# Kernel optimization log

Measured on AMD Instinct MI355X. Metric: run time of the kernel, lower is better.

The kernel has to match this reference:

```python
import jax, jax.numpy as jnp
import numpy as np

LMAX = 4
NC = (LMAX + 1) ** 2          # 25 spherical coefficients
L0 = LMAX + 1                 # number of m=0 coefficients
SPHERE = 128
CIN1 = 2 * SPHERE             # concat(source, target) channels
HID = 64
HEADS = 8
ALPHA_C = 64
VAL_C = 16
OUT_C = 128
GRID = 2 * (LMAX + 1)         # S2 grid resolution
N_NODES = 2500
N_EDGES = 25000
MAX_ELEM = 90
EDGE_IN = 128 + 2 * 64        # distance basis + src/tgt atom embeddings
M_SIZES = [LMAX - m + 1 for m in range(1, LMAX + 1)]  # l-count per |m|>0
RAD_OUT = L0 * CIN1 + sum(s * CIN1 for s in M_SIZES)  # 3840

def _lm(l, m):
    return l * l + l + m
_p = [_lm(l, 0) for l in range(LMAX + 1)]
for m in range(1, LMAX + 1):
    _p += [_lm(l, -m) for l in range(m, LMAX + 1)]
    _p += [_lm(l, m) for l in range(m, LMAX + 1)]
PERM = np.asarray(_p)             # l-primary -> m-primary
INV_PERM = np.argsort(PERM)       # m-primary -> l-primary
EXPAND = np.concatenate([np.full(2 * l + 1, l) for l in range(LMAX + 1)])

def _layernorm(x, g, b, eps=1e-5):
    mu = jnp.mean(x, axis=-1, keepdims=True)
    var = jnp.mean((x - mu) ** 2, axis=-1, keepdims=True)
    return (x - mu) * jax.lax.rsqrt(var + eps) * g + b

def _so2_conv(xm, fc0_w, fc0_b, wms, cin, mout, extra, rad):
    # xm: [E, NC, cin] in m-primary layout. Per-order SO(2) 'complex' conv.
    E = xm.shape[0]
    x0 = xm[:, :L0].reshape(E, L0 * cin)
    off_rad = L0 * cin
    if rad is not None:
        x0 = x0 * rad[:, :off_rad]
    x0 = x0 @ fc0_w + fc0_b
    x0_extra = None
    if extra:
        x0_extra = x0[:, :extra]
        x0 = x0[:, extra:]
    outs = [x0.reshape(E, L0, mout)]
    off = L0
    for i, sz in enumerate(M_SIZES):
        xb = xm[:, off:off + 2 * sz].reshape(E, 2, sz * cin)
        if rad is not None:
            xb = xb * rad[:, off_rad:off_rad + sz * cin][:, None, :]
            off_rad += sz * cin
        y = xb @ wms[i]                         # [E, 2, 2*mout*sz]
        half = y.shape[-1] // 2
        yr, yi = y[..., :half], y[..., half:]
        o = jnp.stack([yr[:, 0] - yi[:, 1], yr[:, 1] + yi[:, 0]], axis=1)
        outs.append(o.reshape(E, 2 * sz, mout))
        off += 2 * sz
    return jnp.concatenate(outs, axis=1), x0_extra

def _segment_softmax(logits, seg, num_segments):
    mx = jax.ops.segment_max(logits, seg, num_segments=num_segments)
    ex = jnp.exp(logits - mx[seg])
    s = jax.ops.segment_sum(ex, seg, num_segments=num_segments)
    return ex / (s[seg] + 1e-16)

def setup_inputs():
    key = jax.random.key(0)
    ks = iter(jax.random.split(key, 64))
    def nrm(shape, scale=1.0):
        return jax.random.normal(next(ks), shape, dtype=jnp.float32) * scale
    def lin(i, o):
        return nrm((i, o), i ** -0.5)
    inp = {}
    inp['x'] = nrm((N_NODES, NC, SPHERE))
    inp['edge_distance'] = nrm((N_EDGES, 128))
    inp['src_table'] = jax.random.uniform(next(ks), (MAX_ELEM, 64), jnp.float32, -0.001, 0.001)
    inp['tgt_table'] = jax.random.uniform(next(ks), (MAX_ELEM, 64), jnp.float32, -0.001, 0.001)
    inp['rad_w1'] = lin(EDGE_IN, 64); inp['rad_b1'] = jnp.zeros((64,), jnp.float32)
    inp['rad_ln1_g'] = jnp.ones((64,), jnp.float32); inp['rad_ln1_b'] = jnp.zeros((64,), jnp.float32)
    inp['rad_w2'] = lin(64, 64); inp['rad_b2'] = jnp.zeros((64,), jnp.float32)
    inp['rad_ln2_g'] = jnp.ones((64,), jnp.float32); inp['rad_ln2_b'] = jnp.zeros((64,), jnp.float32)
    inp['rad_w3'] = lin(64, RAD_OUT); inp['rad_b3'] = jnp.zeros((RAD_OUT,), jnp.float32)
    inp['wigner'] = nrm((N_EDGES, NC, NC), NC ** -0.5)
    extra1 = HEADS * ALPHA_C + HID
    inp['c1_fc0_w'] = lin(L0 * CIN1, L0 * HID + extra1)
    inp['c1_fc0_b'] = jnp.zeros((L0 * HID + extra1,), jnp.float32)
    for i, sz in enumerate(M_SIZES):
        inp['c1_wm%d' % (i + 1)] = lin(sz * CIN1, 2 * HID * sz)
    inp['to_grid'] = nrm((GRID, GRID, NC), NC ** -0.5)
    inp['from_grid'] = nrm((GRID, GRID, NC), float(GRID * GRID) ** -0.5)
    inp['alpha_ln_g'] = jnp.ones((ALPHA_C,), jnp.float32)
    inp['alpha_ln_b'] = jnp.zeros((ALPHA_C,), jnp.float32)
    std = ALPHA_C ** -0.5
    inp['alpha_dot'] = jax.random.uniform(next(ks), (HEADS, ALPHA_C), jnp.float32, -std, std)
    vout = HEADS * VAL_C
    inp['c2_fc0_w'] = lin(L0 * HID, L0 * vout)
    inp['c2_fc0_b'] = jnp.zeros((L0 * vout,), jnp.float32)
    for i, sz in enumerate(M_SIZES):
        inp['c2_wm%d' % (i + 1)] = lin(sz * HID, 2 * vout * sz)
    inp['proj_w'] = nrm((L0, OUT_C, vout), vout ** -0.5)
    inp['proj_b'] = jnp.zeros((OUT_C,), jnp.float32)
    inp['atomic_numbers'] = jax.random.randint(next(ks), (N_NODES,), 0, MAX_ELEM)
    inp['edge_index'] = jax.random.randint(next(ks), (2, N_EDGES), 0, N_NODES)
    return inp

def reference(x, edge_distance, src_table, tgt_table,
              rad_w1, rad_b1, rad_ln1_g, rad_ln1_b, rad_w2, rad_b2, rad_ln2_g, rad_ln2_b, rad_w3, rad_b3,
              wigner, c1_fc0_w, c1_fc0_b, c1_wm1, c1_wm2, c1_wm3, c1_wm4,
              to_grid, from_grid, alpha_ln_g, alpha_ln_b, alpha_dot,
              c2_fc0_w, c2_fc0_b, c2_wm1, c2_wm2, c2_wm3, c2_wm4, proj_w, proj_b,
              atomic_numbers, edge_index):
    E = edge_index.shape[1]
    N = x.shape[0]
    src, tgt = edge_index[0], edge_index[1]
    # invariant edge scalars: distance basis + source/target atom embeddings
    x_edge = jnp.concatenate([edge_distance, src_table[atomic_numbers[src]], tgt_table[atomic_numbers[tgt]]], axis=1)
    # gather node embeddings to edges, rotate into edge frame (Wigner-D)
    msg = jnp.concatenate([x[src], x[tgt]], axis=2)          # [E, NC, 2*SPHERE]
    msg = jnp.einsum('eml,elc->emc', wigner, msg)
    msg = msg[:, PERM]                                        # m-primary layout
    # radial MLP producing per-(m,l,channel) edge weights
    h = jax.nn.silu(_layernorm(x_edge @ rad_w1 + rad_b1, rad_ln1_g, rad_ln1_b))
    h = jax.nn.silu(_layernorm(h @ rad_w2 + rad_b2, rad_ln2_g, rad_ln2_b))
    rad = h @ rad_w3 + rad_b3                                 # [E, RAD_OUT]
    extra1 = HEADS * ALPHA_C + HID
    msg, x0_extra = _so2_conv(msg, c1_fc0_w, c1_fc0_b, (c1_wm1, c1_wm2, c1_wm3, c1_wm4), CIN1, HID, extra1, rad)
    x0_alpha = x0_extra[:, :HEADS * ALPHA_C]
    x0_gate = x0_extra[:, HEADS * ALPHA_C:]
    # separable S2 activation: scalar SiLU on l=0, grid SiLU on l>0
    msg_l = msg[:, INV_PERM]
    grid = jax.nn.silu(jnp.einsum('bai,eic->ebac', to_grid, msg_l))
    s2 = jnp.einsum('bai,ebac->eic', from_grid, grid)
    msg_l = jnp.concatenate([jax.nn.silu(x0_gate)[:, None, :], s2[:, 1:]], axis=1)
    # second SO(2) conv (internal weights, no radial)
    msg_m = msg_l[:, PERM]
    msg_m, _ = _so2_conv(msg_m, c2_fc0_w, c2_fc0_b, (c2_wm1, c2_wm2, c2_wm3, c2_wm4), HID, HEADS * VAL_C, None, None)
    msg_l = msg_m[:, INV_PERM]
    # attention logits (LayerNorm + SmoothLeakyReLU(0.2) + dot)
    a = _layernorm(x0_alpha.reshape(E, HEADS, ALPHA_C), alpha_ln_g, alpha_ln_b)
    a = 0.6 * a + 0.4 * a * (2.0 * jax.nn.sigmoid(a) - 1.0)
    logits = jnp.einsum('ehk,hk->eh', a, alpha_dot)
    # rotate messages back to global frame (wigner_inv = wigner^T)
    msg_l = jnp.einsum('eml,emc->elc', wigner, msg_l)
    alpha = _segment_softmax(logits, tgt, N)                  # [E, HEADS]
    v = msg_l.reshape(E, NC, HEADS, VAL_C) * alpha[:, None, :, None]
    node = jax.ops.segment_sum(v.reshape(E, NC, HEADS * VAL_C), tgt, num_segments=N)
    # SO3_LinearV2 projection: per-degree linear, bias only on l=0
    out = jnp.einsum('nmi,moi->nmo', node, proj_w[EXPAND])
    out = out.at[:, 0, :].add(proj_b)
    return out
```

## Files before the change

kernel.cpp:

```cpp
#include <hip/hip_runtime.h>
#include <cstddef>

typedef unsigned short u16;
typedef __attribute__((ext_vector_type(8))) short short8;
typedef __attribute__((ext_vector_type(4))) float float4v;

__constant__ int c_PERM[25] = {0,2,6,12,20, 1,5,11,19, 3,7,13,21, 4,10,18, 8,14,22, 9,17, 15,23, 16,24};
__constant__ int c_ROFF[25] = {0,256,512,768,1024, 1280,1536,1792,2048, 1280,1536,1792,2048,
                               2304,2560,2816, 2304,2560,2816, 3072,3328, 3072,3328, 3584,3584};
__constant__ int c_EXPAND[25] = {0,1,1,1,2,2,2,2,2,3,3,3,3,3,3,3,4,4,4,4,4,4,4,4,4};

static constexpr int PERM_CE[25] = {0,2,6,12,20, 1,5,11,19, 3,7,13,21, 4,10,18, 8,14,22, 9,17, 15,23, 16,24};
static constexpr int INV_CE[25]  = {0,5,1,9,13, 6,2,10,16,19, 14,7,3,11,17, 21,23,20,15,8, 4,12,18,22,24};

__device__ __forceinline__ float wsum64(float v){
#pragma unroll
  for(int m=32;m>0;m>>=1) v += __shfl_xor(v, m, 64);
  return v;
}
__device__ __forceinline__ float siluf(float x){ return x/(1.f+expf(-x)); }

__device__ __forceinline__ void bsplit(float v, u16 &h, u16 &l){
  unsigned u = __float_as_uint(v);
  unsigned hb = (u + 0x7FFFu + ((u>>16)&1u)) >> 16;
  h = (u16)hb;
  float r = v - __uint_as_float(hb<<16);
  unsigned u2 = __float_as_uint(r);
  l = (u16)((u2 + 0x7FFFu + ((u2>>16)&1u)) >> 16);
}

__global__ __launch_bounds__(256) void wtrans_kernel(const float* __restrict__ W, u16* __restrict__ Wh, u16* __restrict__ Wl, int K, int C2){
  int idx = blockIdx.x*256 + threadIdx.x;
  int K2 = 2*K;
  if(idx >= C2*K2) return;
  int n = idx / K2, k2 = idx % K2;
  int half = C2>>1;
  float v;
  if(k2 < K) v = W[k2*C2 + n];
  else { int k = k2-K; v = (n<half) ? -W[k*C2 + half + n] : W[k*C2 + n - half]; }
  u16 h,l; bsplit(v,h,l);
  Wh[idx]=h; Wl[idx]=l;
}

__global__ __launch_bounds__(256) void fctrans_kernel(const float* __restrict__ W, u16* __restrict__ Wh, u16* __restrict__ Wl, int K, int N){
  int idx = blockIdx.x*256 + threadIdx.x;
  if(idx >= N*K) return;
  int n = idx / K, k = idx % K;
  u16 h,l; bsplit(W[(size_t)k*N + n],h,l);
  Wh[idx]=h; Wl[idx]=l;
}

__global__ __launch_bounds__(256) void ptrans_kernel(const float* __restrict__ pw, float* __restrict__ pwt){
  int idx = blockIdx.x*256+threadIdx.x;
  if(idx >= 5*16384) return;
  int l = idx>>14, r = idx & 16383, i = r>>7, o = r&127;
  pwt[idx] = pw[(l<<14) + (o<<7) + i];
}

__global__ __launch_bounds__(256) void hist_kernel(const int* __restrict__ tgt_all, int* __restrict__ cnt, int E, int C, int NN){
  int idx = blockIdx.x*256+threadIdx.x;
  if(idx>=E) return;
  atomicAdd(&cnt[(idx/C)*NN + tgt_all[idx]], 1);
}
__global__ __launch_bounds__(256) void scan_kernel(const int* __restrict__ cnt, int* __restrict__ basearr, int* __restrict__ cur, int NN, int C){
  int ch = blockIdx.x;
  __shared__ int sh[256];
  __shared__ int carry;
  if(threadIdx.x==0) carry = ch*C;
  __syncthreads();
  for(int t0=0; t0<NN; t0+=256){
    int i = t0 + threadIdx.x;
    int v = (i<NN)? cnt[ch*NN+i] : 0;
    sh[threadIdx.x]=v; __syncthreads();
    for(int off=1; off<256; off<<=1){
      int add = (threadIdx.x>=off)? sh[threadIdx.x-off]:0; __syncthreads();
      sh[threadIdx.x]+=add; __syncthreads();
    }
    int excl = carry + sh[threadIdx.x]-v;
    if(i<NN){ basearr[ch*NN+i]=excl; cur[ch*NN+i]=excl; }
    __syncthreads();
    if(threadIdx.x==255) carry += sh[255];
    __syncthreads();
  }
}
__global__ __launch_bounds__(256) void scatter_kernel(const int* __restrict__ tgt_all, int* __restrict__ cur, int* __restrict__ order, int E, int C, int NN){
  int idx = blockIdx.x*256+threadIdx.x;
  if(idx>=E) return;
  int ch = idx / C;
  int pos = atomicAdd(&cur[ch*NN + tgt_all[idx]], 1);
  order[pos] = idx;
}

__global__ __launch_bounds__(64) void radial_kernel(
    const float* __restrict__ ed, const float* __restrict__ st, const float* __restrict__ tt,
    const float* __restrict__ w1, const float* __restrict__ b1, const float* __restrict__ g1, const float* __restrict__ bb1,
    const float* __restrict__ w2, const float* __restrict__ b2, const float* __restrict__ g2, const float* __restrict__ bb2,
    const int* __restrict__ an, const int* __restrict__ src, const int* __restrict__ tgt,
    u16* __restrict__ h2h, u16* __restrict__ h2l){
  int e = blockIdx.x; int lane = threadIdx.x;
  __shared__ float xe[256];
  __shared__ float h1s[64];
  int s = src[e], t = tgt[e];
  xe[lane]      = ed[(size_t)e*128 + lane];
  xe[64+lane]   = ed[(size_t)e*128 + 64 + lane];
  int as = an[s], at = an[t];
  xe[128+lane]  = st[as*64 + lane];
  xe[192+lane]  = tt[at*64 + lane];
  __syncthreads();
  float acc = b1[lane];
  for(int k=0;k<256;k++) acc += xe[k]*w1[k*64+lane];
  float mu = wsum64(acc)*(1.f/64.f);
  float d = acc - mu;
  float var = wsum64(d*d)*(1.f/64.f);
  float nrm = d*rsqrtf(var+1e-5f)*g1[lane]+bb1[lane];
  h1s[lane] = siluf(nrm);
  __syncthreads();
  float acc2 = b2[lane];
  for(int k=0;k<64;k++) acc2 += h1s[k]*w2[k*64+lane];
  mu = wsum64(acc2)*(1.f/64.f);
  d = acc2-mu;
  var = wsum64(d*d)*(1.f/64.f);
  nrm = d*rsqrtf(var+1e-5f)*g2[lane]+bb2[lane];
  u16 h,l; bsplit(siluf(nrm),h,l);
  h2h[(size_t)e*64+lane]=h; h2l[(size_t)e*64+lane]=l;
}

struct GrpArgs {
  const u16* Ah[6]; const u16* Al[6];
  const u16* Bh[6]; const u16* Bl[6];
  const float* bias[6]; float* C1[6]; float* C2[6];
  int lda[6]; int K[6]; int ldc1[6]; int ldc2[6]; int split[6];
  int xoff[7]; int ng; int M; int gx; int gy;
};

__global__ __launch_bounds__(256) void mgemm_kernel(GrpArgs a){
  __shared__ __align__(16) u16 Ash[2][4096];
  __shared__ __align__(16) u16 Asl[2][4096];
  __shared__ __align__(16) u16 Bsh[2][4096];
  __shared__ __align__(16) u16 Bsl[2][4096];

  int b = blockIdx.x;
  int xcd = b & 7, i = b >> 3;
  int pbase = a.gx >> 3, prem = a.gx & 7;
  int s = pbase + (xcd < prem ? 1 : 0);
  if(i >= s * a.gy) return;
  int o = xcd*pbase + (xcd < prem ? xcd : prem);
  int xt = o + (i % s);
  int yt = i / s;

  int g = 0;
  while(g+1 < a.ng && xt >= a.xoff[g+1]) g++;
  int n0 = (xt - a.xoff[g])*128, m0 = yt*128;
  const int M = a.M, K = a.K[g], lda = a.lda[g];
  const u16* __restrict__ Ah = a.Ah[g]; const u16* __restrict__ Al = a.Al[g];
  const u16* __restrict__ Bh = a.Bh[g]; const u16* __restrict__ Bl = a.Bl[g];
  int t = threadIdx.x;
  int r0 = t>>2, kblk = t&3, k80 = kblk*8;
  int ar0 = m0 + r0; if(ar0 >= M) ar0 = M-1;
  int ar1 = m0 + r0 + 64; if(ar1 >= M) ar1 = M-1;
  const u16* Ap0h = Ah + (size_t)ar0*lda + k80;
  const u16* Ap1h = Ah + (size_t)ar1*lda + k80;
  const u16* Ap0l = Al + (size_t)ar0*lda + k80;
  const u16* Ap1l = Al + (size_t)ar1*lda + k80;
  const u16* Bp0h = Bh + (size_t)(n0+r0)*K + k80;
  const u16* Bp1h = Bh + (size_t)(n0+r0+64)*K + k80;
  const u16* Bp0l = Bl + (size_t)(n0+r0)*K + k80;
  const u16* Bp1l = Bl + (size_t)(n0+r0+64)*K + k80;
  int pcbS = kblk ^ ((r0>>1)&3);
  int sA = r0*32 + pcbS*8;
  int sB = sA + 64*32;

  int wave = t>>6, lane = t&63;
  int wr = wave>>1, wc = wave&1;
  int ml = lane&15, q = lane>>4;
  int pcbA = q ^ ((ml>>1)&3);
  int aoff = (wr*64 + ml)*32 + pcbA*8;
  int boff = (wc*64 + ml)*32 + pcbA*8;

  float4v acc[4][4];
#pragma unroll
  for(int i2=0;i2<4;i2++)
#pragma unroll
    for(int j=0;j<4;j++) acc[i2][j] = 0.f;

  short8 cva[4], cvb[4];
  cva[0] = *(const short8*)(Ap0h); cva[1] = *(const short8*)(Ap1h);
  cva[2] = *(const short8*)(Ap0l); cva[3] = *(const short8*)(Ap1l);
  cvb[0] = *(const short8*)(Bp0h); cvb[1] = *(const short8*)(Bp1h);
  cvb[2] = *(const short8*)(Bp0l); cvb[3] = *(const short8*)(Bp1l);

  int p = 0;
  for(int k0=0; k0<K; k0+=32){
    *(short8*)(&Ash[p][sA]) = cva[0];
    *(short8*)(&Ash[p][sB]) = cva[1];
    *(short8*)(&Asl[p][sA]) = cva[2];
    *(short8*)(&Asl[p][sB]) = cva[3];
    *(short8*)(&Bsh[p][sA]) = cvb[0];
    *(short8*)(&Bsh[p][sB]) = cvb[1];
    *(short8*)(&Bsl[p][sA]) = cvb[2];
    *(short8*)(&Bsl[p][sB]) = cvb[3];
    if(k0+32 < K){
      int kn = k0+32;
      cva[0] = *(const short8*)(Ap0h + kn); cva[1] = *(const short8*)(Ap1h + kn);
      cva[2] = *(const short8*)(Ap0l + kn); cva[3] = *(const short8*)(Ap1l + kn);
      cvb[0] = *(const short8*)(Bp0h + kn); cvb[1] = *(const short8*)(Bp1h + kn);
      cvb[2] = *(const short8*)(Bp0l + kn); cvb[3] = *(const short8*)(Bp1l + kn);
    }
    __syncthreads();
    short8 afh[4], afl[4];
#pragma unroll
    for(int i2=0;i2<4;i2++){
      afh[i2] = *(const short8*)(&Ash[p][aoff + i2*512]);
      afl[i2] = *(const short8*)(&Asl[p][aoff + i2*512]);
    }
#pragma unroll
    for(int j=0;j<4;j++){
      short8 bfh = *(const short8*)(&Bsh[p][boff + j*512]);
      short8 bfl = *(const short8*)(&Bsl[p][boff + j*512]);
#pragma unroll
      for(int i2=0;i2<4;i2++){
        acc[i2][j] = __builtin_amdgcn_mfma_f32_16x16x32_bf16(afh[i2], bfh, acc[i2][j], 0,0,0);
        acc[i2][j] = __builtin_amdgcn_mfma_f32_16x16x32_bf16(afh[i2], bfl, acc[i2][j], 0,0,0);
        acc[i2][j] = __builtin_amdgcn_mfma_f32_16x16x32_bf16(afl[i2], bfh, acc[i2][j], 0,0,0);
      }
    }
    p ^= 1;
  }
  const float* bias = a.bias[g];
  int split = a.split[g];
  float* C1 = a.C1[g]; float* C2 = a.C2[g];
  int ldc1 = a.ldc1[g], ldc2 = a.ldc2[g];
#pragma unroll
  for(int i2=0;i2<4;i2++){
    int rowb = m0 + wr*64 + i2*16 + q*4;
#pragma unroll
    for(int r=0;r<4;r++){
      int row = rowb + r;
      if(row < M){
#pragma unroll
        for(int j=0;j<4;j++){
          int col = n0 + wc*64 + j*16 + ml;
          float v = acc[i2][j][r];
          if(bias) v += bias[col];
          if(col < split) C1[(size_t)row*ldc1 + col] = v;
          else            C2[(size_t)row*ldc2 + (col-split)] = v;
        }
      }
    }
  }
}

__global__ __launch_bounds__(256) void wigner1_kernel(
    const float* __restrict__ x, const float* __restrict__ wigner,
    const int* __restrict__ src, const int* __restrict__ tgt,
    const float* __restrict__ rad, u16* __restrict__ msg1h, u16* __restrict__ msg1l){
  int e = blockIdx.x; int t = threadIdx.x;
  __shared__ float wig[625];
  __shared__ float4 cat4[1600];
  int s = src[e], tg = tgt[e];
  for(int i=t;i<625;i+=256) wig[i] = wigner[(size_t)e*625 + i];
  const float4* xs = (const float4*)(x + (size_t)s*3200);
  const float4* xt = (const float4*)(x + (size_t)tg*3200);
  for(int idx=t; idx<1600; idx+=256){
    int l = idx>>6, slot = idx&63;
    cat4[idx] = (slot<32) ? xs[l*32 + slot] : xt[l*32 + (slot-32)];
  }
  __syncthreads();
  int wave = t>>6, lane = t&63;
  for(int p=wave; p<25; p+=4){
    int pl = c_PERM[p];
    float4 acc = {0.f,0.f,0.f,0.f};
#pragma unroll
    for(int l=0;l<25;l++){
      float w = wig[pl*25 + l];
      float4 c = cat4[l*64 + lane];
      acc.x += w*c.x; acc.y += w*c.y; acc.z += w*c.z; acc.w += w*c.w;
    }
    float4 rd = *(const float4*)(rad + (size_t)e*3840 + c_ROFF[p] + lane*4);
    acc.x*=rd.x; acc.y*=rd.y; acc.z*=rd.z; acc.w*=rd.w;
    u16 h0,h1,h2,h3,l0,l1,l2,l3;
    bsplit(acc.x,h0,l0); bsplit(acc.y,h1,l1); bsplit(acc.z,h2,l2); bsplit(acc.w,h3,l3);
    size_t base = (size_t)e*6400 + p*256 + lane*4;
    *(uint2*)(msg1h + base) = make_uint2((unsigned)h0 | ((unsigned)h1<<16), (unsigned)h2 | ((unsigned)h3<<16));
    *(uint2*)(msg1l + base) = make_uint2((unsigned)l0 | ((unsigned)l1<<16), (unsigned)l2 | ((unsigned)l3<<16));
  }
}

__global__ __launch_bounds__(64) void grid_kernel(
    const float* __restrict__ msg2, const float* __restrict__ x0e,
    const float* __restrict__ tg, const float* __restrict__ fg,
    u16* __restrict__ m2h, u16* __restrict__ m2l){
  int e = blockIdx.x; int lane = threadIdx.x;
  float r[25];
#pragma unroll
  for(int i=0;i<25;i++) r[i] = msg2[((size_t)e*25 + INV_CE[i])*64 + lane];
  float s2[25];
#pragma unroll
  for(int i=0;i<25;i++) s2[i]=0.f;
  for(int g=0; g<100; g++){
    float tv=0.f;
#pragma unroll
    for(int i=0;i<25;i++) tv += tg[g*25+i]*r[i];
    tv = siluf(tv);
#pragma unroll
    for(int i=0;i<25;i++) s2[i] += fg[g*25+i]*tv;
  }
  float gate = siluf(x0e[(size_t)e*576 + 512 + lane]);
#pragma unroll
  for(int p=0;p<25;p++){
    int lp = PERM_CE[p];
    float v = (lp==0) ? gate : s2[lp];
    u16 h,l; bsplit(v,h,l);
    size_t idx = ((size_t)e*25+p)*64 + lane;
    m2h[idx]=h; m2l[idx]=l;
  }
}

__global__ __launch_bounds__(64) void alpha_kernel(
    const float* __restrict__ x0e, const float* __restrict__ g, const float* __restrict__ b,
    const float* __restrict__ adot, const int* __restrict__ tgt,
    float* __restrict__ exb, float* __restrict__ ssum){
  int e = blockIdx.x; int lane = threadIdx.x;
  int t = tgt[e];
  float gg = g[lane], bb = b[lane];
  for(int h=0;h<8;h++){
    float v = x0e[(size_t)e*576 + h*64 + lane];
    float mu = wsum64(v)*(1.f/64.f);
    float d = v-mu;
    float var = wsum64(d*d)*(1.f/64.f);
    float a = d*rsqrtf(var+1e-5f)*gg+bb;
    float sig = 1.f/(1.f+expf(-a));
    float a2 = 0.6f*a + 0.4f*a*(2.f*sig-1.f);
    float p = a2*adot[h*64+lane];
    float lg = wsum64(p);
    if(lane==0){
      float ex = expf(lg);
      exb[e*8+h]=ex;
      atomicAdd(&ssum[t*8+h], ex);
    }
  }
}

__global__ __launch_bounds__(256) void agg_kernel(
    const float* __restrict__ wigner_all, const float* __restrict__ msg3,
    const float* __restrict__ exb, const int* __restrict__ order,
    const int* __restrict__ basearr, const int* __restrict__ cnt,
    float* __restrict__ node, int e0){
  int n = blockIdx.x; int t = threadIdx.x;
  int lg = t>>5;
  int c4 = t&31;
  __shared__ float wig2[625];
  __shared__ float m3s[3200];
  float4v acc[4];
#pragma unroll
  for(int k=0;k<4;k++) acc[k] = 0.f;
  float* nb = node + (size_t)n*3200;
#pragma unroll
  for(int k=0;k<4;k++){ int l = lg + 8*k; if(l<25) acc[k] = *(const float4v*)(nb + l*128 + c4*4); }
  int nE = cnt[n], b0 = basearr[n];
  for(int j=0;j<nE;j++){
    int e = order[b0+j];
    int el = e - e0;
    __syncthreads();
    for(int i=t;i<625;i+=256){ int q=i/25, l=i%25; wig2[i] = wigner_all[((size_t)e*25 + c_PERM[q])*25 + l]; }
    for(int i=t;i<800;i+=256) ((float4*)m3s)[i] = ((const float4*)(msg3 + (size_t)el*3200))[i];
    __syncthreads();
    float ex = exb[el*8 + (c4>>2)];
    float4v tmp[4];
#pragma unroll
    for(int k=0;k<4;k++) tmp[k] = 0.f;
    for(int q=0;q<25;q++){
      float4v m = *(const float4v*)(m3s + q*128 + c4*4);
#pragma unroll
      for(int k=0;k<4;k++){
        int l = lg + 8*k;
        float w = (l<25) ? wig2[q*25 + l] : 0.f;
        tmp[k] += w*m;
      }
    }
#pragma unroll
    for(int k=0;k<4;k++) acc[k] += ex*tmp[k];
  }
#pragma unroll
  for(int k=0;k<4;k++){ int l = lg + 8*k; if(l<25) *(float4v*)(nb + l*128 + c4*4) = acc[k]; }
}

__global__ __launch_bounds__(256) void proj_kernel(
    const float* __restrict__ node, const float* __restrict__ ssum,
    const float* __restrict__ pwt, const float* __restrict__ proj_b,
    float* __restrict__ out, int NN){
  int n0 = blockIdx.x*2; int t = threadIdx.x;
  __shared__ float nd[2][3200];
  __shared__ float inv[2][8];
  if(t<16){
    int j=t>>3, h=t&7;
    int n=n0+j; if(n>=NN) n=NN-1;
    inv[j][h] = 1.f/(ssum[n*8+h] + 1e-16f);
  }
  __syncthreads();
  int n1 = (n0+1 < NN) ? (n0+1) : (NN-1);
  for(int i=t;i<3200;i+=256){
    int h = (i&127)>>4;
    nd[0][i] = node[(size_t)n0*3200 + i] * inv[0][h];
    nd[1][i] = node[(size_t)n1*3200 + i] * inv[1][h];
  }
  __syncthreads();
  int o = t&127, half = t>>7;
  for(int p=half;p<25;p+=2){
    int l = c_EXPAND[p];
    const float* w = pwt + l*16384;
    float a0=0.f, a1=0.f;
    for(int i=0;i<128;i++){
      float wv = w[i*128+o];
      a0 += nd[0][p*128+i]*wv;
      a1 += nd[1][p*128+i]*wv;
    }
    float bs = (p==0)? proj_b[o] : 0.f;
    out[((size_t)n0*25+p)*128 + o] = a0 + bs;
    if(n0+1 < NN) out[((size_t)(n0+1)*25+p)*128 + o] = a1 + bs;
  }
}

extern "C" void kernel_launch(void* const* d_in, const int* in_sizes, int n_in,
                              void* d_out, int out_size, void* d_ws, size_t ws_size,
                              hipStream_t stream) {
  const float* x           = (const float*)d_in[0];
  const float* edge_dist   = (const float*)d_in[1];
  const float* src_table   = (const float*)d_in[2];
  const float* tgt_table   = (const float*)d_in[3];
  const float* rad_w1      = (const float*)d_in[4];
  const float* rad_b1      = (const float*)d_in[5];
  const float* rad_ln1_g   = (const float*)d_in[6];
  const float* rad_ln1_b   = (const float*)d_in[7];
  const float* rad_w2      = (const float*)d_in[8];
  const float* rad_b2      = (const float*)d_in[9];
  const float* rad_ln2_g   = (const float*)d_in[10];
  const float* rad_ln2_b   = (const float*)d_in[11];
  const float* rad_w3      = (const float*)d_in[12];
  const float* rad_b3      = (const float*)d_in[13];
  const float* wigner      = (const float*)d_in[14];
  const float* c1_fc0_w    = (const float*)d_in[15];
  const float* c1_fc0_b    = (const float*)d_in[16];
  const float* c1_wm[4]    = {(const float*)d_in[17],(const float*)d_in[18],(const float*)d_in[19],(const float*)d_in[20]};
  const float* to_grid     = (const float*)d_in[21];
  const float* from_grid   = (const float*)d_in[22];
  const float* alpha_ln_g  = (const float*)d_in[23];
  const float* alpha_ln_b  = (const float*)d_in[24];
  const float* alpha_dot   = (const float*)d_in[25];
  const float* c2_fc0_w    = (const float*)d_in[26];
  const float* c2_fc0_b    = (const float*)d_in[27];
  const float* c2_wm[4]    = {(const float*)d_in[28],(const float*)d_in[29],(const float*)d_in[30],(const float*)d_in[31]};
  const float* proj_w      = (const float*)d_in[32];
  const float* proj_b      = (const float*)d_in[33];
  const int*   atomic_nums = (const int*)d_in[34];
  const int*   edge_index  = (const int*)d_in[35];
  float* out = (float*)d_out;
  (void)n_in; (void)out_size;

  const int E  = in_sizes[35]/2;
  const int NN = in_sizes[34];

  const int K1[4] = {1024, 768, 512, 256}, C1c[4] = {512, 384, 256, 128};
  const int K2[4] = {256, 192, 128, 64},  C2c[4] = {1024, 768, 512, 256};
  const size_t W3T = 3840*64;
  const size_t FC1 = 896*1280;
  const size_t W1S[4] = {512*2048, 384*1536, 256*1024, 128*512};
  const size_t FC2 = 640*320;
  const size_t W2S[4] = {1024*512, 768*384, 512*256, 256*128};
  size_t wush = 2*(W3T + FC1 + W1S[0]+W1S[1]+W1S[2]+W1S[3] + FC2 + W2S[0]+W2S[1]+W2S[2]+W2S[3]);
  const size_t persist = (size_t)NN*8 + (size_t)NN*3200 + wush/2 + 81920 + 8192;
  const size_t wfl = ws_size / sizeof(float);
  const int copts[10] = {25000, 12500, 6250, 5000, 3125, 2500, 1250, 625, 250, 125};
  int C = 125;
  for(int i=0;i<10;i++){
    size_t nchI = (size_t)((E + copts[i]-1)/copts[i]);
    size_t hc = (size_t)(copts[i]+1)/2;
    size_t need = (size_t)copts[i]*(6400+576+8) + hc*3840 + persist + 3*nchI*NN + E;
    if(need <= wfl){ C = copts[i]; break; }
  }
  const int nch = (E + C - 1)/C;
  const size_t halfC = (size_t)(C+1)/2;

  float* ws = (float*)d_ws;
  u16* msg1h = (u16*)ws;
  u16* msg1l = msg1h + (size_t)C*6400;
  u16* m2h   = (u16*)ws;
  u16* m2l   = m2h + (size_t)C*1600;
  float* msg3 = ws + (size_t)C*1600;
  float* rad  = ws + (size_t)C*6400;
  float* msg2 = rad;
  float* x0e  = rad + halfC*3840;
  u16* h2h = (u16*)x0e;
  u16* h2l = h2h + halfC*64;
  float* exb  = x0e + (size_t)C*576;
  float* ssum = exb + (size_t)C*8;
  float* node = ssum + (size_t)NN*8;
  u16* wb = (u16*)(node + (size_t)NN*3200);
  u16 *w3h = wb, *w3l = w3h + W3T;
  u16 *f1h = w3l + W3T, *f1l = f1h + FC1;
  u16 *w1h[4], *w1l[4];
  u16* p = f1l + FC1;
  for(int i=0;i<4;i++){ w1h[i]=p; w1l[i]=p+W1S[i]; p += 2*W1S[i]; }
  u16 *f2h = p, *f2l = f2h + FC2; p = f2l + FC2;
  u16 *w2h[4], *w2l[4];
  for(int i=0;i<4;i++){ w2h[i]=p; w2l[i]=p+W2S[i]; p += 2*W2S[i]; }
  float* pwt = (float*)p;
  int* cntb  = (int*)(pwt + 81920);
  int* baseb = cntb + (size_t)nch*NN;
  int* curb  = baseb + (size_t)nch*NN;
  int* order = curb + (size_t)nch*NN;

  hipMemsetAsync(node, 0, (size_t)NN*3200*sizeof(float), stream);
  hipMemsetAsync(ssum, 0, (size_t)NN*8*sizeof(float), stream);
  hipMemsetAsync(cntb, 0, (size_t)nch*NN*sizeof(int), stream);

  const int* tgt_all = edge_index + E;
  hist_kernel<<<(E+255)/256, 256, 0, stream>>>(tgt_all, cntb, E, C, NN);
  scan_kernel<<<nch, 256, 0, stream>>>(cntb, baseb, curb, NN, C);
  scatter_kernel<<<(E+255)/256, 256, 0, stream>>>(tgt_all, curb, order, E, C, NN);

  fctrans_kernel<<<((int)W3T+255)/256, 256, 0, stream>>>(rad_w3, w3h, w3l, 64, 3840);
  fctrans_kernel<<<((int)FC1+255)/256, 256, 0, stream>>>(c1_fc0_w, f1h, f1l, 1280, 896);
  fctrans_kernel<<<((int)FC2+255)/256, 256, 0, stream>>>(c2_fc0_w, f2h, f2l, 320, 640);
  for(int i=0;i<4;i++)
    wtrans_kernel<<<((int)W1S[i]*2+255)/256, 256, 0, stream>>>(c1_wm[i], w1h[i], w1l[i], K1[i], C1c[i]);
  for(int i=0;i<4;i++)
    wtrans_kernel<<<((int)W2S[i]*2+255)/256, 256, 0, stream>>>(c2_wm[i], w2h[i], w2l[i], K2[i], C2c[i]);
  ptrans_kernel<<<320, 256, 0, stream>>>(proj_w, pwt);

  auto launchM = [&](GrpArgs &ga, int gx, int gy){
    ga.gx = gx; ga.gy = gy;
    int base = gx>>3, rem = gx&7;
    int maxs = base + (rem?1:0);
    mgemm_kernel<<<8*maxs*gy, 256, 0, stream>>>(ga);
  };

  const int OFF1[4] = {5,13,19,23};
  for(int ch=0; ch<nch; ch++){
    int e0 = ch*C;
    int ce = (E - e0 < C) ? (E - e0) : C;
    const int* srcp = edge_index + e0;
    const int* tgtp = edge_index + E + e0;
    const float* wigp = wigner + (size_t)e0*625;
    int mt = (ce+127)/128;

    int half1 = (ce+1)/2;
    for(int hh=0; hh<2; hh++){
      int h0 = hh ? half1 : 0;
      int he = hh ? (ce - half1) : half1;
      if(he <= 0) continue;
      radial_kernel<<<he, 64, 0, stream>>>(edge_dist + (size_t)(e0+h0)*128, src_table, tgt_table,
          rad_w1, rad_b1, rad_ln1_g, rad_ln1_b, rad_w2, rad_b2, rad_ln2_g, rad_ln2_b,
          atomic_nums, srcp+h0, tgtp+h0, h2h, h2l);
      {
        GrpArgs ga = {};
        ga.ng = 1; ga.M = he;
        ga.Ah[0]=h2h; ga.Al[0]=h2l; ga.Bh[0]=w3h; ga.Bl[0]=w3l;
        ga.bias[0]=rad_b3; ga.C1[0]=rad; ga.C2[0]=nullptr;
        ga.lda[0]=64; ga.K[0]=64; ga.ldc1[0]=3840; ga.ldc2[0]=0; ga.split[0]=3840;
        ga.xoff[0]=0; ga.xoff[1]=30;
        launchM(ga, 30, (he+127)/128);
      }
      wigner1_kernel<<<he, 256, 0, stream>>>(x, wigp + (size_t)h0*625, srcp+h0, tgtp+h0, rad,
          msg1h + (size_t)h0*6400, msg1l + (size_t)h0*6400);
    }

    {
      GrpArgs ga = {};
      ga.ng = 5; ga.M = ce;
      ga.Ah[0]=msg1h; ga.Al[0]=msg1l; ga.Bh[0]=f1h; ga.Bl[0]=f1l;
      ga.bias[0]=c1_fc0_b; ga.C1[0]=x0e; ga.C2[0]=msg2;
      ga.lda[0]=6400; ga.K[0]=1280; ga.ldc1[0]=576; ga.ldc2[0]=1600; ga.split[0]=576;
      int xo = 7;
      ga.xoff[0]=0; ga.xoff[1]=7;
      for(int i=0;i<4;i++){
        int gidx = i+1;
        ga.Ah[gidx]=msg1h + (size_t)OFF1[i]*256; ga.Al[gidx]=msg1l + (size_t)OFF1[i]*256;
        ga.Bh[gidx]=w1h[i]; ga.Bl[gidx]=w1l[i];
        ga.bias[gidx]=nullptr; ga.C1[gidx]=msg2 + OFF1[i]*64; ga.C2[gidx]=nullptr;
        ga.lda[gidx]=6400; ga.K[gidx]=2*K1[i]; ga.ldc1[gidx]=1600; ga.ldc2[gidx]=0; ga.split[gidx]=C1c[i];
        xo += C1c[i]/128;
        ga.xoff[gidx+1]=xo;
      }
      launchM(ga, xo, mt);
    }

    grid_kernel<<<ce, 64, 0, stream>>>(msg2, x0e, to_grid, from_grid, m2h, m2l);
    alpha_kernel<<<ce, 64, 0, stream>>>(x0e, alpha_ln_g, alpha_ln_b, alpha_dot, tgtp, exb, ssum);

    {
      GrpArgs ga = {};
      ga.ng = 5; ga.M = ce;
      ga.Ah[0]=m2h; ga.Al[0]=m2l; ga.Bh[0]=f2h; ga.Bl[0]=f2l;
      ga.bias[0]=c2_fc0_b; ga.C1[0]=msg3; ga.C2[0]=nullptr;
      ga.lda[0]=1600; ga.K[0]=320; ga.ldc1[0]=3200; ga.ldc2[0]=0; ga.split[0]=640;
      int xo = 5;
      ga.xoff[0]=0; ga.xoff[1]=5;
      for(int i=0;i<4;i++){
        int gidx = i+1;
        ga.Ah[gidx]=m2h + (size_t)OFF1[i]*64; ga.Al[gidx]=m2l + (size_t)OFF1[i]*64;
        ga.Bh[gidx]=w2h[i]; ga.Bl[gidx]=w2l[i];
        ga.bias[gidx]=nullptr; ga.C1[gidx]=msg3 + OFF1[i]*128; ga.C2[gidx]=nullptr;
        ga.lda[gidx]=1600; ga.K[gidx]=2*K2[i]; ga.ldc1[gidx]=3200; ga.ldc2[gidx]=0; ga.split[gidx]=C2c[i];
        xo += C2c[i]/128;
        ga.xoff[gidx+1]=xo;
      }
      launchM(ga, xo, mt);
    }

    agg_kernel<<<NN, 256, 0, stream>>>(wigner, msg3, exb, order,
        baseb + (size_t)ch*NN, cntb + (size_t)ch*NN, node, e0);
  }

  proj_kernel<<<(NN+1)/2, 256, 0, stream>>>(node, ssum, pwt, proj_b, out, NN);
}
```

Baseline: 3.585 ms.

## Process edges in global target-sorted order and skip empty nodes in aggregation

Result: no change. 3.540 ms (-1.2%).

```diff
diff --git a/kernel.cpp b/kernel.cpp
--- a/kernel.cpp
+++ b/kernel.cpp
@@ -57,52 +57,56 @@
   pwt[idx] = pw[(l<<14) + (o<<7) + i];
 }
 
-__global__ __launch_bounds__(256) void hist_kernel(const int* __restrict__ tgt_all, int* __restrict__ cnt, int E, int C, int NN){
+__global__ __launch_bounds__(256) void hist_kernel(const int* __restrict__ tgt_all, int* __restrict__ cnt, int E){
   int idx = blockIdx.x*256+threadIdx.x;
   if(idx>=E) return;
-  atomicAdd(&cnt[(idx/C)*NN + tgt_all[idx]], 1);
-}
-__global__ __launch_bounds__(256) void scan_kernel(const int* __restrict__ cnt, int* __restrict__ basearr, int* __restrict__ cur, int NN, int C){
-  int ch = blockIdx.x;
+  atomicAdd(&cnt[tgt_all[idx]], 1);
+}
+__global__ __launch_bounds__(256) void scan_kernel(const int* __restrict__ cnt, int* __restrict__ basearr, int* __restrict__ cur, int NN){
   __shared__ int sh[256];
   __shared__ int carry;
-  if(threadIdx.x==0) carry = ch*C;
+  if(threadIdx.x==0) carry = 0;
   __syncthreads();
   for(int t0=0; t0<NN; t0+=256){
     int i = t0 + threadIdx.x;
-    int v = (i<NN)? cnt[ch*NN+i] : 0;
+    int v = (i<NN)? cnt[i] : 0;
     sh[threadIdx.x]=v; __syncthreads();
     for(int off=1; off<256; off<<=1){
       int add = (threadIdx.x>=off)? sh[threadIdx.x-off]:0; __syncthreads();
       sh[threadIdx.x]+=add; __syncthreads();
     }
     int excl = carry + sh[threadIdx.x]-v;
-    if(i<NN){ basearr[ch*NN+i]=excl; cur[ch*NN+i]=excl; }
+    if(i<NN){ basearr[i]=excl; cur[i]=excl; }
     __syncthreads();
     if(threadIdx.x==255) carry += sh[255];
     __syncthreads();
   }
 }
-__global__ __launch_bounds__(256) void scatter_kernel(const int* __restrict__ tgt_all, int* __restrict__ cur, int* __restrict__ order, int E, int C, int NN){
+__global__ __launch_bounds__(256) void scatter_kernel(const int* __restrict__ ei, int* __restrict__ cur,
+    int* __restrict__ order, int* __restrict__ srcs, int* __restrict__ tgts, int E){
   int idx = blockIdx.x*256+threadIdx.x;
   if(idx>=E) return;
-  int ch = idx / C;
-  int pos = atomicAdd(&cur[ch*NN + tgt_all[idx]], 1);
+  int t = ei[E+idx];
+  int pos = atomicAdd(&cur[t], 1);
   order[pos] = idx;
+  tgts[pos] = t;
+  srcs[pos] = ei[idx];
 }
 
 __global__ __launch_bounds__(64) void radial_kernel(
     const float* __restrict__ ed, const float* __restrict__ st, const float* __restrict__ tt,
     const float* __restrict__ w1, const float* __restrict__ b1, const float* __restrict__ g1, const float* __restrict__ bb1,
     const float* __restrict__ w2, const float* __restrict__ b2, const float* __restrict__ g2, const float* __restrict__ bb2,
-    const int* __restrict__ an, const int* __restrict__ src, const int* __restrict__ tgt,
+    const int* __restrict__ an, const int* __restrict__ order,
+    const int* __restrict__ src, const int* __restrict__ tgt,
     u16* __restrict__ h2h, u16* __restrict__ h2l){
   int e = blockIdx.x; int lane = threadIdx.x;
   __shared__ float xe[256];
   __shared__ float h1s[64];
+  int eo = order[e];
   int s = src[e], t = tgt[e];
-  xe[lane]      = ed[(size_t)e*128 + lane];
-  xe[64+lane]   = ed[(size_t)e*128 + 64 + lane];
+  xe[lane]      = ed[(size_t)eo*128 + lane];
+  xe[64+lane]   = ed[(size_t)eo*128 + 64 + lane];
   int as = an[s], at = an[t];
   xe[128+lane]  = st[as*64 + lane];
   xe[192+lane]  = tt[at*64 + lane];
@@ -199,6 +203,7 @@
     *(short8*)(&Bsh[p][sB]) = cvb[1];
     *(short8*)(&Bsl[p][sA]) = cvb[2];
     *(short8*)(&Bsl[p][sB]) = cvb[3];
+    __syncthreads();
     if(k0+32 < K){
       int kn = k0+32;
       cva[0] = *(const short8*)(Ap0h + kn); cva[1] = *(const short8*)(Ap1h + kn);
@@ -206,7 +211,6 @@
       cvb[0] = *(const short8*)(Bp0h + kn); cvb[1] = *(const short8*)(Bp1h + kn);
       cvb[2] = *(const short8*)(Bp0l + kn); cvb[3] = *(const short8*)(Bp1l + kn);
     }
-    __syncthreads();
     short8 afh[4], afl[4];
 #pragma unroll
     for(int i2=0;i2<4;i2++){
@@ -251,14 +255,15 @@
 }
 
 __global__ __launch_bounds__(256) void wigner1_kernel(
-    const float* __restrict__ x, const float* __restrict__ wigner,
-    const int* __restrict__ src, const int* __restrict__ tgt,
+    const float* __restrict__ x, const float* __restrict__ wigner_all,
+    const int* __restrict__ order, const int* __restrict__ src, const int* __restrict__ tgt,
     const float* __restrict__ rad, u16* __restrict__ msg1h, u16* __restrict__ msg1l){
   int e = blockIdx.x; int t = threadIdx.x;
   __shared__ float wig[625];
   __shared__ float4 cat4[1600];
+  int eo = order[e];
   int s = src[e], tg = tgt[e];
-  for(int i=t;i<625;i+=256) wig[i] = wigner[(size_t)e*625 + i];
+  for(int i=t;i<625;i+=256) wig[i] = wigner_all[(size_t)eo*625 + i];
   const float4* xs = (const float4*)(x + (size_t)s*3200);
   const float4* xt = (const float4*)(x + (size_t)tg*3200);
   for(int idx=t; idx<1600; idx+=256){
@@ -345,8 +350,12 @@
     const float* __restrict__ wigner_all, const float* __restrict__ msg3,
     const float* __restrict__ exb, const int* __restrict__ order,
     const int* __restrict__ basearr, const int* __restrict__ cnt,
-    float* __restrict__ node, int e0){
+    float* __restrict__ node, int e0, int e1){
   int n = blockIdx.x; int t = threadIdx.x;
+  int b0 = basearr[n], c = cnt[n];
+  int lo = b0 > e0 ? b0 : e0;
+  int hi = (b0+c) < e1 ? (b0+c) : e1;
+  if(lo >= hi) return;
   int lg = t>>5;
   int c4 = t&31;
   __shared__ float wig2[625];
@@ -357,10 +366,9 @@
   float* nb = node + (size_t)n*3200;
 #pragma unroll
   for(int k=0;k<4;k++){ int l = lg + 8*k; if(l<25) acc[k] = *(const float4v*)(nb + l*128 + c4*4); }
-  int nE = cnt[n], b0 = basearr[n];
-  for(int j=0;j<nE;j++){
-    int e = order[b0+j];
-    int el = e - e0;
+  for(int j=lo;j<hi;j++){
+    int e = order[j];
+    int el = j - e0;
     __syncthreads();
     for(int i=t;i<625;i+=256){ int q=i/25, l=i%25; wig2[i] = wigner_all[((size_t)e*25 + c_PERM[q])*25 + l]; }
     for(int i=t;i<800;i+=256) ((float4*)m3s)[i] = ((const float4*)(msg3 + (size_t)el*3200))[i];
@@ -467,15 +475,15 @@
   const size_t W1S[4] = {512*2048, 384*1536, 256*1024, 128*512};
   const size_t FC2 = 640*320;
   const size_t W2S[4] = {1024*512, 768*384, 512*256, 256*128};
-  size_t wush = 2*(W3T + FC1 + W1S[0]+W1S[1]+W1S[2]+W1S[3] + FC2 + W2S[0]+W2S[1]+W2S[2]+W2S[3]);
-  const size_t persist = (size_t)NN*8 + (size_t)NN*3200 + wush/2 + 81920 + 8192;
+  const size_t WSUM = W3T + FC1 + W1S[0]+W1S[1]+W1S[2]+W1S[3] + FC2 + W2S[0]+W2S[1]+W2S[2]+W2S[3];
+  const size_t persist = (size_t)NN*8 + (size_t)NN*3200 + WSUM
+                       + 81920 + (size_t)3*NN + (size_t)3*E + 8192;
   const size_t wfl = ws_size / sizeof(float);
   const int copts[10] = {25000, 12500, 6250, 5000, 3125, 2500, 1250, 625, 250, 125};
   int C = 125;
   for(int i=0;i<10;i++){
-    size_t nchI = (size_t)((E + copts[i]-1)/copts[i]);
     size_t hc = (size_t)(copts[i]+1)/2;
-    size_t need = (size_t)copts[i]*(6400+576+8) + hc*3840 + persist + 3*nchI*NN + E;
+    size_t need = (size_t)copts[i]*(6400+576+8) + hc*3840 + persist;
     if(need <= wfl){ C = copts[i]; break; }
   }
   const int nch = (E + C - 1)/C;
@@ -506,18 +514,19 @@
   for(int i=0;i<4;i++){ w2h[i]=p; w2l[i]=p+W2S[i]; p += 2*W2S[i]; }
   float* pwt = (float*)p;
   int* cntb  = (int*)(pwt + 81920);
-  int* baseb = cntb + (size_t)nch*NN;
-  int* curb  = baseb + (size_t)nch*NN;
-  int* order = curb + (size_t)nch*NN;
+  int* baseb = cntb + NN;
+  int* curb  = baseb + NN;
+  int* order = curb + NN;
+  int* srcs  = order + E;
+  int* tgts  = srcs + E;
 
   hipMemsetAsync(node, 0, (size_t)NN*3200*sizeof(float), stream);
   hipMemsetAsync(ssum, 0, (size_t)NN*8*sizeof(float), stream);
-  hipMemsetAsync(cntb, 0, (size_t)nch*NN*sizeof(int), stream);
-
-  const int* tgt_all = edge_index + E;
-  hist_kernel<<<(E+255)/256, 256, 0, stream>>>(tgt_all, cntb, E, C, NN);
-  scan_kernel<<<nch, 256, 0, stream>>>(cntb, baseb, curb, NN, C);
-  scatter_kernel<<<(E+255)/256, 256, 0, stream>>>(tgt_all, curb, order, E, C, NN);
+  hipMemsetAsync(cntb, 0, (size_t)NN*sizeof(int), stream);
+
+  hist_kernel<<<(E+255)/256, 256, 0, stream>>>(edge_index + E, cntb, E);
+  scan_kernel<<<1, 256, 0, stream>>>(cntb, baseb, curb, NN);
+  scatter_kernel<<<(E+255)/256, 256, 0, stream>>>(edge_index, curb, order, srcs, tgts, E);
 
   fctrans_kernel<<<((int)W3T+255)/256, 256, 0, stream>>>(rad_w3, w3h, w3l, 64, 3840);
   fctrans_kernel<<<((int)FC1+255)/256, 256, 0, stream>>>(c1_fc0_w, f1h, f1l, 1280, 896);
@@ -539,9 +548,6 @@
   for(int ch=0; ch<nch; ch++){
     int e0 = ch*C;
     int ce = (E - e0 < C) ? (E - e0) : C;
-    const int* srcp = edge_index + e0;
-    const int* tgtp = edge_index + E + e0;
-    const float* wigp = wigner + (size_t)e0*625;
     int mt = (ce+127)/128;
 
     int half1 = (ce+1)/2;
@@ -549,9 +555,9 @@
       int h0 = hh ? half1 : 0;
       int he = hh ? (ce - half1) : half1;
       if(he <= 0) continue;
-      radial_kernel<<<he, 64, 0, stream>>>(edge_dist + (size_t)(e0+h0)*128, src_table, tgt_table,
+      radial_kernel<<<he, 64, 0, stream>>>(edge_dist, src_table, tgt_table,
           rad_w1, rad_b1, rad_ln1_g, rad_ln1_b, rad_w2, rad_b2, rad_ln2_g, rad_ln2_b,
-          atomic_nums, srcp+h0, tgtp+h0, h2h, h2l);
+          atomic_nums, order + e0 + h0, srcs + e0 + h0, tgts + e0 + h0, h2h, h2l);
       {
         GrpArgs ga = {};
         ga.ng = 1; ga.M = he;
@@ -561,8 +567,8 @@
         ga.xoff[0]=0; ga.xoff[1]=30;
         launchM(ga, 30, (he+127)/128);
       }
-      wigner1_kernel<<<he, 256, 0, stream>>>(x, wigp + (size_t)h0*625, srcp+h0, tgtp+h0, rad,
-          msg1h + (size_t)h0*6400, msg1l + (size_t)h0*6400);
+      wigner1_kernel<<<he, 256, 0, stream>>>(x, wigner, order + e0 + h0, srcs + e0 + h0, tgts + e0 + h0,
+          rad, msg1h + (size_t)h0*6400, msg1l + (size_t)h0*6400);
     }
 
     {
@@ -586,7 +592,7 @@
     }
 
     grid_kernel<<<ce, 64, 0, stream>>>(msg2, x0e, to_grid, from_grid, m2h, m2l);
-    alpha_kernel<<<ce, 64, 0, stream>>>(x0e, alpha_ln_g, alpha_ln_b, alpha_dot, tgtp, exb, ssum);
+    alpha_kernel<<<ce, 64, 0, stream>>>(x0e, alpha_ln_g, alpha_ln_b, alpha_dot, tgts + e0, exb, ssum);
 
     {
       GrpArgs ga = {};
@@ -608,8 +614,7 @@
       launchM(ga, xo, mt);
     }
 
-    agg_kernel<<<NN, 256, 0, stream>>>(wigner, msg3, exb, order,
-        baseb + (size_t)ch*NN, cntb + (size_t)ch*NN, node, e0);
+    agg_kernel<<<NN, 256, 0, stream>>>(wigner, msg3, exb, order, baseb, cntb, node, e0, e0+ce);
   }
 
   proj_kernel<<<(NN+1)/2, 256, 0, stream>>>(node, ssum, pwt, proj_b, out, NN);
```
